# Optimization experiments

Hardware: AMD Instinct MI355X
Metric: run time of the kernel (lower is better)

The kernel has to match this reference:

```python
import jax, jax.numpy as jnp
import numpy as np

SL, BS, HS, FFN = 2048, 1, 512, 2048
E, TOP_K = 8, 2


def setup_inputs() -> dict:
    key = jax.random.key(0)
    k_x, k_w, k_i, k_w1, k_w2 = jax.random.split(key, 5)
    x = jax.random.normal(k_x, (SL, BS, HS), dtype=jnp.float32)
    expert_weights = jax.random.uniform(k_w, (SL * BS, TOP_K), dtype=jnp.float32)
    expert_indices = jax.random.randint(k_i, (SL * BS, TOP_K), 0, E, dtype=jnp.int32)
    # grouped expert MLP params (megablocks GroupedMLP, regular type, no bias)
    w1 = jax.random.normal(k_w1, (E, HS, FFN), dtype=jnp.float32) * (HS ** -0.5)
    w2 = jax.random.normal(k_w2, (E, FFN, HS), dtype=jnp.float32) * (FFN ** -0.5)
    return {"x": x, "expert_weights": expert_weights, "expert_indices": expert_indices,
            "w1": w1, "w2": w2}


def reference(x, expert_weights, expert_indices, w1, w2):
    sl, bs, hs = x.shape
    n_tok = sl * bs
    xf = x.reshape(n_tok, hs)                      # [N, hs]
    ew = expert_weights.reshape(-1)                # [N*top_k]
    ei = expert_indices.reshape(-1)                # [N*top_k]

    # indices_and_bins: stable radix sort of assignments by expert id
    indices = jnp.argsort(ei)                      # stable in jax -> sorted assignment ids
    bin_ids = ei[indices]                          # sorted expert id per assignment

    # megablocks gather: row for assignment i is indices[i] // top_k
    rows = indices // TOP_K                        # [T]
    xg = xf[rows]                                  # [T, hs] expert-contiguous tokens

    # grouped GEMM expert MLP (dense masked loop over fixed expert count)
    outg = jnp.zeros_like(xg)
    for e in range(E):
        m = (bin_ids == e).astype(x.dtype)[:, None]
        h = jax.nn.gelu(xg @ w1[e], approximate=False)   # [T, ffn]
        outg = outg + m * (h @ w2[e])                    # [T, hs]

    # buffer.index_add_(0, E*input_indices + bin_ids, output.detach())
    buf_idx = E * rows + bin_ids
    buffer = jnp.zeros((n_tok * E, hs), x.dtype).at[buf_idx].add(
        jax.lax.stop_gradient(outg))

    # megablocks scatter: weighted combine back to token order
    y = jnp.zeros((n_tok, hs), x.dtype).at[rows].add(outg * ew[indices][:, None])
    return y.reshape(sl, bs, hs), buffer.reshape(n_tok, E, hs)
```

## Files before the change

### kernel.cpp

```cpp
#include <hip/hip_runtime.h>
#include <hip/hip_bf16.h>

#define NTOK 2048
#define TOPK 2
#define HS   512
#define FFN  2048
#define NE   8
#define TASSIGN (NTOK*TOPK)
#define PAD  5120
#define MAXT128 40
#define MAXT64  72

typedef __attribute__((ext_vector_type(8))) short bf16x8;
typedef __attribute__((ext_vector_type(4))) float f32x4;

static const size_t OFF_XBF  = 0;
static const size_t OFF_W1T  = 2097152;
static const size_t OFF_W2T  = 18874368;
static const size_t OFF_H    = 35651584;
static const size_t OFF_OUTV = 56623104;
static const size_t OFF_RT   = 67108864;
static const size_t OFF_HROF = 67129344;
static const size_t OFF_TE128= 67145728;
static const size_t OFF_TR128= 67145888;
static const size_t OFF_TE64 = 67146048;
static const size_t OFF_TR64 = 67146336;

__device__ __forceinline__ unsigned short f2bf(float f) {
    union { __hip_bfloat16 h; unsigned short u; } v;
    v.h = __float2bfloat16(f);
    return v.u;
}

__device__ __forceinline__ int swz(int r, int byte_off) {
    return byte_off ^ ((r & 7) << 4);
}

#define GLOAD16(gsrc, ldst) \
    __builtin_amdgcn_global_load_lds((const __attribute__((address_space(1))) void*)(gsrc), \
                                     (__attribute__((address_space(3))) void*)(ldst), 16, 0, 0)

__device__ __forceinline__ void dev_transpose(const float* __restrict__ in,
                                              unsigned short* __restrict__ out,
                                              int R, int C, int e, int rb, int cb, int tid) {
    __shared__ unsigned short t[32][33];
    int tx = tid & 31, ty = tid >> 5;
    const float* ip = in + (size_t)e * R * C;
    unsigned short* op = out + (size_t)e * C * R;
#pragma unroll
    for (int i = 0; i < 4; i++) {
        int r = ty + i * 8;
        t[r][tx] = f2bf(ip[(size_t)(rb + r) * C + cb + tx]);
    }
    __syncthreads();
#pragma unroll
    for (int i = 0; i < 4; i++) {
        int c = ty + i * 8;
        op[(size_t)(cb + c) * R + rb + tx] = t[tx][c];
    }
}

__global__ __launch_bounds__(256) void k_prep(
        const float* __restrict__ x, const float* __restrict__ w1,
        const float* __restrict__ w2, const int* __restrict__ ei,
        unsigned short* __restrict__ xbf, unsigned short* __restrict__ w1T,
        unsigned short* __restrict__ w2T,
        int* __restrict__ rowtok, int* __restrict__ hrof,
        int* __restrict__ te128, int* __restrict__ tr128,
        int* __restrict__ te64, int* __restrict__ tr64) {
    int b = blockIdx.x;
    int tid = threadIdx.x;
    if (b == 0) {
        __shared__ int cnt[NE], offpad[NE], cur[NE];
        for (int i = tid; i < PAD; i += 256) rowtok[i] = 0;
        if (tid < NE) cnt[tid] = 0;
        __syncthreads();
        for (int a = tid; a < TASSIGN; a += 256) atomicAdd(&cnt[ei[a]], 1);
        __syncthreads();
        if (tid == 0) {
            int o = 0, t1 = 0, t2 = 0;
            for (int e = 0; e < NE; e++) {
                offpad[e] = o; cur[e] = 0;
                for (int r = 0; r < cnt[e]; r += 128) { te128[t1] = e; tr128[t1] = o + r; t1++; }
                for (int r = 0; r < cnt[e]; r += 64)  { te64[t2]  = e; tr64[t2]  = o + r; t2++; }
                o += (cnt[e] + 127) / 128 * 128;
            }
            for (; t1 < MAXT128; t1++) te128[t1] = -1;
            for (; t2 < MAXT64;  t2++) te64[t2]  = -1;
        }
        __syncthreads();
        for (int a = tid; a < TASSIGN; a += 256) {
            int e = ei[a];
            int r = atomicAdd(&cur[e], 1);
            int hr = offpad[e] + r;
            rowtok[hr] = a >> 1;
            hrof[a] = hr;
        }
    } else if (b < 1 + 1024) {
        int i = ((b - 1) * 256 + tid) * 4;
        float4 v = *(const float4*)(x + i);
        ushort4 o;
        o.x = f2bf(v.x); o.y = f2bf(v.y); o.z = f2bf(v.z); o.w = f2bf(v.w);
        *(ushort4*)(xbf + i) = o;
    } else if (b < 1 + 1024 + 8192) {
        int blk = b - 1025;
        int e = blk >> 10, rem = blk & 1023;
        dev_transpose(w1, w1T, HS, FFN, e, (rem >> 6) * 32, (rem & 63) * 32, tid);
    } else {
        int blk = b - 9217;
        int e = blk >> 10, rem = blk & 1023;
        dev_transpose(w2, w2T, FFN, HS, e, (rem >> 4) * 32, (rem & 15) * 32, tid);
    }
}

template<int BM, int BN, int K, bool G1>
__global__ __launch_bounds__(256) void k_gemm(
        const unsigned short* __restrict__ A,
        const unsigned short* __restrict__ B,
        void* __restrict__ outp,
        const int* __restrict__ rowtok,
        const int* __restrict__ te, const int* __restrict__ tr, int N) {
    constexpr int MI = BM / 32, NJ = BN / 32;
    constexpr int PA = BM / 32, PB = BN / 32;
    constexpr int ABYTES = BM * 64 * 2, BBYTES = BN * 64 * 2;
    constexpr int NSTEP = K / 64;
    static_assert(NSTEP % 2 == 0, "even steps");

    int mt = blockIdx.y;
    int e = te[mt];
    if (e < 0) return;
    int hr0 = tr[mt];
    int ct = blockIdx.x;

    __shared__ int4 ldsv[(2 * (ABYTES + BBYTES)) / 16];
    char* A0 = (char*)ldsv;
    char* A1 = A0 + ABYTES;
    char* B0 = A1 + ABYTES;
    char* B1 = B0 + BBYTES;

    int tid = threadIdx.x;
    int lane = tid & 63, wave = tid >> 6;
    int wm = wave >> 1, wn = wave & 1;

    const char* asrc[PA];
    const char* bsrc[PB];
    int adoff[PA], bdoff[PB];
#pragma unroll
    for (int p = 0; p < PA; p++) {
        int idx = p * 256 + tid;
        int r = idx >> 3, c8 = idx & 7;
        int c8s = c8 ^ (r & 7);
        size_t row = G1 ? (size_t)rowtok[hr0 + r] : (size_t)(hr0 + r);
        asrc[p] = (const char*)(A + row * K) + c8s * 16;
        adoff[p] = (p * 256 + wave * 64) * 16;
    }
#pragma unroll
    for (int p = 0; p < PB; p++) {
        int idx = p * 256 + tid;
        int r = idx >> 3, c8 = idx & 7;
        int c8s = c8 ^ (r & 7);
        bsrc[p] = (const char*)(B + ((size_t)e * N + (size_t)ct * BN + r) * K) + c8s * 16;
        bdoff[p] = (p * 256 + wave * 64) * 16;
    }

    f32x4 acc[MI][NJ] = {};

    auto stage = [&](char* Ad, char* Bd, int s) {
        int kb = s * 128;
#pragma unroll
        for (int p = 0; p < PA; p++) GLOAD16(asrc[p] + kb, Ad + adoff[p]);
#pragma unroll
        for (int p = 0; p < PB; p++) GLOAD16(bsrc[p] + kb, Bd + bdoff[p]);
    };
    auto compute = [&](const char* As, const char* Bs) {
#pragma unroll
        for (int kk = 0; kk < 64; kk += 32) {
            bf16x8 af[MI], bfv[NJ];
#pragma unroll
            for (int i = 0; i < MI; i++) {
                int ar = wm * (BM / 2) + i * 16 + (lane & 15);
                af[i] = *(const bf16x8*)(As + swz(ar, ar * 128 + kk * 2 + (lane >> 4) * 16));
            }
#pragma unroll
            for (int j = 0; j < NJ; j++) {
                int bc = wn * (BN / 2) + j * 16 + (lane & 15);
                bfv[j] = *(const bf16x8*)(Bs + swz(bc, bc * 128 + kk * 2 + (lane >> 4) * 16));
            }
#pragma unroll
            for (int i = 0; i < MI; i++)
#pragma unroll
                for (int j = 0; j < NJ; j++)
                    acc[i][j] = __builtin_amdgcn_mfma_f32_16x16x32_bf16(af[i], bfv[j], acc[i][j], 0, 0, 0);
        }
    };

    stage(A0, B0, 0);
    __syncthreads();
#pragma unroll 1
    for (int s = 0; s < NSTEP; s += 2) {
        if (s + 1 < NSTEP) stage(A1, B1, s + 1);
        compute(A0, B0);
        __syncthreads();
        if (s + 2 < NSTEP) stage(A0, B0, s + 2);
        compute(A1, B1);
        __syncthreads();
    }

    if constexpr (G1) {
        unsigned short* O = (unsigned short*)outp;
#pragma unroll
        for (int i = 0; i < MI; i++)
#pragma unroll
            for (int j = 0; j < NJ; j++)
#pragma unroll
                for (int q = 0; q < 4; q++) {
                    int row = hr0 + wm * (BM / 2) + i * 16 + (lane >> 4) * 4 + q;
                    int col = ct * BN + wn * (BN / 2) + j * 16 + (lane & 15);
                    float v = acc[i][j][q];
                    float g = 0.5f * v * (1.0f + erff(v * 0.70710678118f));
                    O[(size_t)row * N + col] = f2bf(g);
                }
    } else {
        float* O = (float*)outp;
#pragma unroll
        for (int i = 0; i < MI; i++)
#pragma unroll
            for (int j = 0; j < NJ; j++)
#pragma unroll
                for (int q = 0; q < 4; q++) {
                    int row = hr0 + wm * (BM / 2) + i * 16 + (lane >> 4) * 4 + q;
                    int col = ct * BN + wn * (BN / 2) + j * 16 + (lane & 15);
                    O[(size_t)row * N + col] = acc[i][j][q];
                }
    }
}

__global__ __launch_bounds__(256) void k_combine(
        const float4* __restrict__ outv, const int* __restrict__ ei,
        const float* __restrict__ ew, const int* __restrict__ hrof,
        float4* __restrict__ y, float4* __restrict__ buf) {
    int g = blockIdx.x * 256 + threadIdx.x;
    int t = g >> 7, c4 = g & 127;
    int a0 = 2 * t, a1 = a0 + 1;
    int h0 = hrof[a0], h1 = hrof[a1];
    float4 o0 = outv[(size_t)h0 * (HS / 4) + c4];
    float4 o1 = outv[(size_t)h1 * (HS / 4) + c4];
    float w0 = ew[a0], w1 = ew[a1];
    y[g] = make_float4(w0 * o0.x + w1 * o1.x, w0 * o0.y + w1 * o1.y,
                       w0 * o0.z + w1 * o1.z, w0 * o0.w + w1 * o1.w);
    int e0 = ei[a0], e1 = ei[a1];
    size_t base = (size_t)t * (NE * HS / 4) + c4;
#pragma unroll
    for (int e = 0; e < NE; e++) {
        float4 v = make_float4(0.f, 0.f, 0.f, 0.f);
        if (e == e0) { v.x += o0.x; v.y += o0.y; v.z += o0.z; v.w += o0.w; }
        if (e == e1) { v.x += o1.x; v.y += o1.y; v.z += o1.z; v.w += o1.w; }
        buf[base + (size_t)e * (HS / 4)] = v;
    }
}

extern "C" void kernel_launch(void* const* d_in, const int* in_sizes, int n_in,
                              void* d_out, int out_size, void* d_ws, size_t ws_size,
                              hipStream_t stream) {
    const float* x  = (const float*)d_in[0];
    const float* ew = (const float*)d_in[1];
    const int*   ei = (const int*)d_in[2];
    const float* w1 = (const float*)d_in[3];
    const float* w2 = (const float*)d_in[4];

    char* ws = (char*)d_ws;
    unsigned short* xbf  = (unsigned short*)(ws + OFF_XBF);
    unsigned short* w1T  = (unsigned short*)(ws + OFF_W1T);
    unsigned short* w2T  = (unsigned short*)(ws + OFF_W2T);
    unsigned short* Hb   = (unsigned short*)(ws + OFF_H);
    float*          outv = (float*)(ws + OFF_OUTV);
    int*            rowtok = (int*)(ws + OFF_RT);
    int*            hrof   = (int*)(ws + OFF_HROF);
    int*            te128  = (int*)(ws + OFF_TE128);
    int*            tr128  = (int*)(ws + OFF_TR128);
    int*            te64   = (int*)(ws + OFF_TE64);
    int*            tr64   = (int*)(ws + OFF_TR64);

    float* y   = (float*)d_out;
    float* buf = (float*)d_out + (size_t)NTOK * HS;

    k_prep<<<1 + 1024 + 8192 + 8192, 256, 0, stream>>>(
        x, w1, w2, ei, xbf, w1T, w2T, rowtok, hrof, te128, tr128, te64, tr64);
    k_gemm<128, 64, HS, true><<<dim3(FFN / 64, MAXT128), 256, 0, stream>>>(
        xbf, w1T, Hb, rowtok, te128, tr128, FFN);
    k_gemm<64, 64, FFN, false><<<dim3(HS / 64, MAXT64), 256, 0, stream>>>(
        Hb, w2T, outv, rowtok, te64, tr64, HS);
    k_combine<<<NTOK * HS / 4 / 256, 256, 0, stream>>>(
        (const float4*)outv, ei, ew, hrof, (float4*)y, (float4*)buf);
}
```

Measured before the change: 86.73 us.

## Split-K the second expert GEMM, store bf16 partials, use fast tanh GELU

The second grouped GEMM now splits its K dimension (FFN) in two across blockIdx.z. This doubles the block count so the GPU is filled better. Each split writes its partial result as bf16 to a separate region, and the combine kernel sums the two partials while doing the weighted scatter with 8-wide vectors. The first GEMM's exact erf GELU is replaced with a tanh-style sigmoid approximation built on __expf, which cuts epilogue cost but changes numerics. Rounding the partials to bf16 also loses some precision.

```diff
diff --git a/kernel.cpp b/kernel.cpp
--- a/kernel.cpp
+++ b/kernel.cpp
@@ -12,6 +12,7 @@
 #define MAXT64  72
 
 typedef __attribute__((ext_vector_type(8))) short bf16x8;
+typedef __attribute__((ext_vector_type(8))) unsigned short u16x8;
 typedef __attribute__((ext_vector_type(4))) float f32x4;
 
 static const size_t OFF_XBF  = 0;
@@ -32,8 +33,20 @@
     return v.u;
 }
 
+__device__ __forceinline__ float bf2f(unsigned short u) {
+    union { unsigned int i; float f; } v;
+    v.i = ((unsigned int)u) << 16;
+    return v.f;
+}
+
 __device__ __forceinline__ int swz(int r, int byte_off) {
     return byte_off ^ ((r & 7) << 4);
+}
+
+__device__ __forceinline__ float gelu_fast(float x) {
+    float z2 = x * fmaf(0.0713548162726f, x * x, 1.5957691216057f);
+    float e = __expf(z2);
+    return x - __fdividef(x, e + 1.0f);
 }
 
 #define GLOAD16(gsrc, ldst) \
@@ -113,17 +126,17 @@
     }
 }
 
-template<int BM, int BN, int K, bool G1>
+template<int BM, int BN, int KFULL, int KLOC, bool G1>
 __global__ __launch_bounds__(256) void k_gemm(
         const unsigned short* __restrict__ A,
         const unsigned short* __restrict__ B,
-        void* __restrict__ outp,
+        unsigned short* __restrict__ outp,
         const int* __restrict__ rowtok,
         const int* __restrict__ te, const int* __restrict__ tr, int N) {
     constexpr int MI = BM / 32, NJ = BN / 32;
     constexpr int PA = BM / 32, PB = BN / 32;
     constexpr int ABYTES = BM * 64 * 2, BBYTES = BN * 64 * 2;
-    constexpr int NSTEP = K / 64;
+    constexpr int NSTEP = KLOC / 64;
     static_assert(NSTEP % 2 == 0, "even steps");
 
     int mt = blockIdx.y;
@@ -131,6 +144,8 @@
     if (e < 0) return;
     int hr0 = tr[mt];
     int ct = blockIdx.x;
+    int kz = blockIdx.z;
+    int k0 = kz * KLOC;
 
     __shared__ int4 ldsv[(2 * (ABYTES + BBYTES)) / 16];
     char* A0 = (char*)ldsv;
@@ -151,7 +166,7 @@
         int r = idx >> 3, c8 = idx & 7;
         int c8s = c8 ^ (r & 7);
         size_t row = G1 ? (size_t)rowtok[hr0 + r] : (size_t)(hr0 + r);
-        asrc[p] = (const char*)(A + row * K) + c8s * 16;
+        asrc[p] = (const char*)(A + row * KFULL + k0) + c8s * 16;
         adoff[p] = (p * 256 + wave * 64) * 16;
     }
 #pragma unroll
@@ -159,7 +174,7 @@
         int idx = p * 256 + tid;
         int r = idx >> 3, c8 = idx & 7;
         int c8s = c8 ^ (r & 7);
-        bsrc[p] = (const char*)(B + ((size_t)e * N + (size_t)ct * BN + r) * K) + c8s * 16;
+        bsrc[p] = (const char*)(B + ((size_t)e * N + (size_t)ct * BN + r) * KFULL + k0) + c8s * 16;
         bdoff[p] = (p * 256 + wave * 64) * 16;
     }
 
@@ -207,7 +222,6 @@
     }
 
     if constexpr (G1) {
-        unsigned short* O = (unsigned short*)outp;
 #pragma unroll
         for (int i = 0; i < MI; i++)
 #pragma unroll
@@ -216,12 +230,10 @@
                 for (int q = 0; q < 4; q++) {
                     int row = hr0 + wm * (BM / 2) + i * 16 + (lane >> 4) * 4 + q;
                     int col = ct * BN + wn * (BN / 2) + j * 16 + (lane & 15);
-                    float v = acc[i][j][q];
-                    float g = 0.5f * v * (1.0f + erff(v * 0.70710678118f));
-                    O[(size_t)row * N + col] = f2bf(g);
+                    outp[(size_t)row * N + col] = f2bf(gelu_fast(acc[i][j][q]));
                 }
     } else {
-        float* O = (float*)outp;
+        unsigned short* O = outp + (size_t)kz * PAD * HS;
 #pragma unroll
         for (int i = 0; i < MI; i++)
 #pragma unroll
@@ -230,32 +242,46 @@
                 for (int q = 0; q < 4; q++) {
                     int row = hr0 + wm * (BM / 2) + i * 16 + (lane >> 4) * 4 + q;
                     int col = ct * BN + wn * (BN / 2) + j * 16 + (lane & 15);
-                    O[(size_t)row * N + col] = acc[i][j][q];
+                    O[(size_t)row * N + col] = f2bf(acc[i][j][q]);
                 }
     }
 }
 
 __global__ __launch_bounds__(256) void k_combine(
-        const float4* __restrict__ outv, const int* __restrict__ ei,
+        const unsigned short* __restrict__ outv, const int* __restrict__ ei,
         const float* __restrict__ ew, const int* __restrict__ hrof,
-        float4* __restrict__ y, float4* __restrict__ buf) {
+        float* __restrict__ y, float* __restrict__ buf) {
+    constexpr size_t SPLIT = (size_t)PAD * HS;
     int g = blockIdx.x * 256 + threadIdx.x;
-    int t = g >> 7, c4 = g & 127;
+    int t = g >> 6, c8 = g & 63;
     int a0 = 2 * t, a1 = a0 + 1;
     int h0 = hrof[a0], h1 = hrof[a1];
-    float4 o0 = outv[(size_t)h0 * (HS / 4) + c4];
-    float4 o1 = outv[(size_t)h1 * (HS / 4) + c4];
+    u16x8 q0a = *(const u16x8*)(outv + (size_t)h0 * HS + c8 * 8);
+    u16x8 q0b = *(const u16x8*)(outv + SPLIT + (size_t)h0 * HS + c8 * 8);
+    u16x8 q1a = *(const u16x8*)(outv + (size_t)h1 * HS + c8 * 8);
+    u16x8 q1b = *(const u16x8*)(outv + SPLIT + (size_t)h1 * HS + c8 * 8);
     float w0 = ew[a0], w1 = ew[a1];
-    y[g] = make_float4(w0 * o0.x + w1 * o1.x, w0 * o0.y + w1 * o1.y,
-                       w0 * o0.z + w1 * o1.z, w0 * o0.w + w1 * o1.w);
+    float o0[8], o1[8], yy[8];
+#pragma unroll
+    for (int k = 0; k < 8; k++) {
+        o0[k] = bf2f(q0a[k]) + bf2f(q0b[k]);
+        o1[k] = bf2f(q1a[k]) + bf2f(q1b[k]);
+        yy[k] = w0 * o0[k] + w1 * o1[k];
+    }
+    float* yp = y + (size_t)t * HS + c8 * 8;
+    *(float4*)(yp)     = make_float4(yy[0], yy[1], yy[2], yy[3]);
+    *(float4*)(yp + 4) = make_float4(yy[4], yy[5], yy[6], yy[7]);
     int e0 = ei[a0], e1 = ei[a1];
-    size_t base = (size_t)t * (NE * HS / 4) + c4;
+    float* bt = buf + (size_t)t * (NE * HS) + c8 * 8;
 #pragma unroll
     for (int e = 0; e < NE; e++) {
-        float4 v = make_float4(0.f, 0.f, 0.f, 0.f);
-        if (e == e0) { v.x += o0.x; v.y += o0.y; v.z += o0.z; v.w += o0.w; }
-        if (e == e1) { v.x += o1.x; v.y += o1.y; v.z += o1.z; v.w += o1.w; }
-        buf[base + (size_t)e * (HS / 4)] = v;
+        float v[8];
+#pragma unroll
+        for (int k = 0; k < 8; k++)
+            v[k] = (e == e0 ? o0[k] : 0.0f) + (e == e1 ? o1[k] : 0.0f);
+        float* be = bt + (size_t)e * HS;
+        *(float4*)(be)     = make_float4(v[0], v[1], v[2], v[3]);
+        *(float4*)(be + 4) = make_float4(v[4], v[5], v[6], v[7]);
     }
 }
 
@@ -273,7 +299,7 @@
     unsigned short* w1T  = (unsigned short*)(ws + OFF_W1T);
     unsigned short* w2T  = (unsigned short*)(ws + OFF_W2T);
     unsigned short* Hb   = (unsigned short*)(ws + OFF_H);
-    float*          outv = (float*)(ws + OFF_OUTV);
+    unsigned short* outv = (unsigned short*)(ws + OFF_OUTV);
     int*            rowtok = (int*)(ws + OFF_RT);
     int*            hrof   = (int*)(ws + OFF_HROF);
     int*            te128  = (int*)(ws + OFF_TE128);
@@ -286,10 +312,10 @@
 
     k_prep<<<1 + 1024 + 8192 + 8192, 256, 0, stream>>>(
         x, w1, w2, ei, xbf, w1T, w2T, rowtok, hrof, te128, tr128, te64, tr64);
-    k_gemm<128, 64, HS, true><<<dim3(FFN / 64, MAXT128), 256, 0, stream>>>(
+    k_gemm<128, 64, HS, HS, true><<<dim3(FFN / 64, MAXT128), 256, 0, stream>>>(
         xbf, w1T, Hb, rowtok, te128, tr128, FFN);
-    k_gemm<64, 64, FFN, false><<<dim3(HS / 64, MAXT64), 256, 0, stream>>>(
+    k_gemm<64, 64, FFN, FFN / 2, false><<<dim3(HS / 64, MAXT64, 2), 256, 0, stream>>>(
         Hb, w2T, outv, rowtok, te64, tr64, HS);
-    k_combine<<<NTOK * HS / 4 / 256, 256, 0, stream>>>(
-        (const float4*)outv, ei, ew, hrof, (float4*)y, (float4*)buf);
-}
+    k_combine<<<NTOK * HS / 8 / 256, 256, 0, stream>>>(
+        outv, ei, ew, hrof, y, buf);
+}
```

Measured after the change: 88.65 us. 2.2% more time.
